# Kernel tuning notes

Measured on AMD Instinct MI355X. Metric: run time of the kernel, lower is better.

## Reference

```python
import jax, jax.numpy as jnp
import numpy as np

DIM = 512
HEADS = 4
MARGIN = 1.0


def _attn_pool(x, Wq, bq, Wk, bk, Wv, bv, Wo, bo):
    # SelfAttention(video_dim, m_dim=DIM, heads=HEADS) followed by mean over time
    B, T, _ = x.shape
    hd = DIM // HEADS
    q = (x @ Wq + bq).reshape(B, T, HEADS, hd)
    k = (x @ Wk + bk).reshape(B, T, HEADS, hd)
    v = (x @ Wv + bv).reshape(B, T, HEADS, hd)
    a = jax.nn.softmax(jnp.einsum('bthd,bshd->bhts', q, k) / jnp.sqrt(jnp.float32(hd)), axis=-1)
    out = jnp.einsum('bhts,bshd->bthd', a, v).reshape(B, T, DIM) @ Wo + bo
    return out.mean(axis=1)  # [B, DIM]


def _ranking(x1, x2, gmask, margin):
    # vectorized form of the per-row torch.roll loop:
    # s[i, b] = <x1[b], x2[(b - i) mod B]>
    B = x1.shape[0]
    idx = (jnp.arange(B)[None, :] - jnp.arange(B)[:, None]) % B  # [B, B]
    s = jnp.einsum('bc,ibc->ib', x1, x2[idx])                    # [B, B]
    mask = gmask[idx] & gmask[None, :]                           # [B, B]
    # max-margin ranking loss with per-column masked mean, then mean over valid cols
    loss = jnp.maximum(0.0, margin + s[1:] - s[0:1])             # [B-1, B]
    m = mask[1:]
    cnt = m.sum(axis=0)
    col_mean = jnp.where(cnt > 0, (loss * m).sum(axis=0) / jnp.maximum(cnt, 1), 0.0)
    valid = cnt > 0
    loss_val = jnp.sum(col_mean * valid) / jnp.maximum(valid.sum(), 1)
    # ranking accuracy: idx==0 iff the true (row 0) score is max among selected
    sel_sum = jnp.sum(jnp.where(mask, s, 0.0), axis=0)
    col_valid = (sel_sum != 0) & mask.any(axis=0)
    s_masked = jnp.where(mask, s, -jnp.inf)
    top_is_first = (s[0] >= s_masked.max(axis=0)).astype(jnp.float32)
    acc = jnp.sum(jnp.where(col_valid, top_is_first, 0.0)) / jnp.maximum(col_valid.sum(), 1)
    return loss_val, jax.lax.stop_gradient(acc)


def setup_inputs() -> dict:
    key = jax.random.key(0)
    ks = iter(jax.random.split(key, 64))

    def nrm(shape, s=0.02):
        return jax.random.normal(next(ks), shape, jnp.float32) * s

    inp = {
        'o': jax.random.normal(next(ks), (128, 1024, DIM), jnp.float32),
        'rgb': jax.random.normal(next(ks), (128, 64, 2048), jnp.float32),
        'audio': jax.random.normal(next(ks), (128, 64, 128), jnp.float32),
        'group_mask': jax.random.randint(next(ks), (128,), 0, 2).astype(bool),
    }
    for name, d in (('rgb', 2048), ('audio', 128)):
        inp[f'{name}_Wq'] = nrm((d, DIM)); inp[f'{name}_bq'] = jnp.zeros((DIM,), jnp.float32)
        inp[f'{name}_Wk'] = nrm((d, DIM)); inp[f'{name}_bk'] = jnp.zeros((DIM,), jnp.float32)
        inp[f'{name}_Wv'] = nrm((d, DIM)); inp[f'{name}_bv'] = jnp.zeros((DIM,), jnp.float32)
        inp[f'{name}_Wo'] = nrm((DIM, DIM)); inp[f'{name}_bo'] = jnp.zeros((DIM,), jnp.float32)
        inp[f'{name}_W2'] = nrm((DIM, DIM)); inp[f'{name}_b2'] = jnp.zeros((DIM,), jnp.float32)
    inp['expand_W'] = nrm((DIM, 2 * DIM))
    inp['expand_b'] = jnp.zeros((2 * DIM,), jnp.float32)
    return inp


def reference(o, rgb, audio, group_mask,
              rgb_Wq, rgb_bq, rgb_Wk, rgb_bk, rgb_Wv, rgb_bv, rgb_Wo, rgb_bo, rgb_W2, rgb_b2,
              audio_Wq, audio_bq, audio_Wk, audio_bk, audio_Wv, audio_bv, audio_Wo, audio_bo,
              audio_W2, audio_b2, expand_W, expand_b):
    # per-modality encoders (CollaborativeGating multiplies are discarded in the
    # original forward, so gating is a no-op on the output -> skipped)
    f_rgb = _attn_pool(rgb, rgb_Wq, rgb_bq, rgb_Wk, rgb_bk, rgb_Wv, rgb_bv, rgb_Wo, rgb_bo) @ rgb_W2 + rgb_b2
    f_aud = _attn_pool(audio, audio_Wq, audio_bq, audio_Wk, audio_bk, audio_Wv, audio_bv, audio_Wo, audio_bo) @ audio_W2 + audio_b2
    feat = jnp.concatenate([f_rgb, f_aud], axis=-1)  # [B, 2*DIM]
    oo = o.mean(axis=-2) @ expand_W + expand_b       # [B, 2*DIM]
    oo = oo / jnp.maximum(jnp.linalg.norm(oo, axis=-1, keepdims=True), 1e-12)
    l1, a1 = _ranking(oo, feat, group_mask, MARGIN)
    l2, a2 = _ranking(feat, oo, group_mask, MARGIN)
    loss = l1 + l2
    acc = (a1 + a2) / 2.0
    return loss, acc
```

## Files before the change

### kernel.cpp

```cpp
#include <hip/hip_runtime.h>
#include <hip/hip_bf16.h>
#include <math.h>


using bf16x8 = __attribute__((ext_vector_type(8))) __bf16;
using f32x4  = __attribute__((ext_vector_type(4))) float;

enum : size_t {
  B_PART = 0,
  B_OM   = B_PART + (size_t)128*32*512*4,
  B_OO   = B_OM   + (size_t)128*512*4,
  B_G    = B_OO   + (size_t)128*1024*4,
  B_PP   = B_G    + (size_t)128*128*4,
  B_PO   = B_PP   + (size_t)2*128*512*4,
  B_FEAT = B_PO   + (size_t)2*128*512*4,
  B_QBF  = B_FEAT + (size_t)2*128*512*4,
  B_KBF  = B_QBF  + (size_t)2*8192*512*2,
  B_VF   = B_KBF  + (size_t)2*8192*512*2,
  B_XBF  = B_VF   + (size_t)2*8192*512*4,
  B_WT   = B_XBF  + (size_t)8192*2048*2,
  B_END  = B_WT   + (size_t)3*512*2048*2
};

__global__ __launch_bounds__(256) void mean_partial_k(const float* __restrict__ o,
                                                      float* __restrict__ part) {
  int c = blockIdx.x, b = blockIdx.y;
  const float* base = o + ((size_t)b * 1024 + (size_t)c * 64) * 512;
  int d4 = (threadIdx.x & 127) << 2;
  int half = threadIdx.x >> 7;
  float4 s = {0.f, 0.f, 0.f, 0.f};
  for (int t = half; t < 64; t += 2) {
    float4 v = *(const float4*)(base + (size_t)t * 512 + d4);
    s.x += v.x; s.y += v.y; s.z += v.z; s.w += v.w;
  }
  *(float4*)(part + (((size_t)b * 16 + c) * 2 + half) * 512 + d4) = s;
}

__global__ __launch_bounds__(512) void finalize_mean_k(const float* __restrict__ part,
                                                       float* __restrict__ om) {
  int b = blockIdx.x, d = threadIdx.x;
  float s = 0.f;
  for (int c = 0; c < 32; ++c) s += part[((size_t)b * 32 + c) * 512 + d];
  om[(size_t)b * 512 + d] = s * (1.f / 1024.f);
}

__global__ __launch_bounds__(256) void gemm_f32_k(
    const float* __restrict__ A, int lda,
    const float* __restrict__ W, int ldw,
    const float* __restrict__ bias,
    float* __restrict__ C, int ldc, int K) {
  __shared__ float As[16][65];
  __shared__ float Ws[16][64];
  int tid = threadIdx.x;
  int tx = tid & 15, ty = tid >> 4;
  int row0 = blockIdx.y * 64, col0 = blockIdx.x * 64;
  float acc[4][4] = {};
  int ar = tid >> 2, ac = (tid & 3) << 2;
  int wr = tid >> 4, wc = (tid & 15) << 2;
  for (int k0 = 0; k0 < K; k0 += 16) {
    float4 av = *(const float4*)(A + (size_t)(row0 + ar) * lda + k0 + ac);
    As[ac + 0][ar] = av.x; As[ac + 1][ar] = av.y;
    As[ac + 2][ar] = av.z; As[ac + 3][ar] = av.w;
    float4 wv = *(const float4*)(W + (size_t)(k0 + wr) * ldw + col0 + wc);
    *(float4*)&Ws[wr][wc] = wv;
    __syncthreads();
#pragma unroll
    for (int k = 0; k < 16; ++k) {
      float a0 = As[k][(ty << 2) + 0], a1 = As[k][(ty << 2) + 1];
      float a2 = As[k][(ty << 2) + 2], a3 = As[k][(ty << 2) + 3];
      float4 w = *(const float4*)&Ws[k][tx << 2];
      acc[0][0] += a0 * w.x; acc[0][1] += a0 * w.y; acc[0][2] += a0 * w.z; acc[0][3] += a0 * w.w;
      acc[1][0] += a1 * w.x; acc[1][1] += a1 * w.y; acc[1][2] += a1 * w.z; acc[1][3] += a1 * w.w;
      acc[2][0] += a2 * w.x; acc[2][1] += a2 * w.y; acc[2][2] += a2 * w.z; acc[2][3] += a2 * w.w;
      acc[3][0] += a3 * w.x; acc[3][1] += a3 * w.y; acc[3][2] += a3 * w.z; acc[3][3] += a3 * w.w;
    }
    __syncthreads();
  }
  float4 bv = *(const float4*)(bias + col0 + (tx << 2));
#pragma unroll
  for (int i = 0; i < 4; ++i) {
    float4 ov;
    ov.x = acc[i][0] + bv.x; ov.y = acc[i][1] + bv.y;
    ov.z = acc[i][2] + bv.z; ov.w = acc[i][3] + bv.w;
    *(float4*)(C + (size_t)(row0 + (ty << 2) + i) * ldc + col0 + (tx << 2)) = ov;
  }
}

__global__ __launch_bounds__(256) void gemm_f32_2w_k(
    const float* __restrict__ A,
    const float* __restrict__ W0, const float* __restrict__ W1,
    const float* __restrict__ b0, const float* __restrict__ b1,
    float* __restrict__ C) {
  const float* W = (blockIdx.y >= 2) ? W1 : W0;
  const float* bias = (blockIdx.y >= 2) ? b1 : b0;
  __shared__ float As[16][65];
  __shared__ float Ws[16][64];
  int tid = threadIdx.x;
  int tx = tid & 15, ty = tid >> 4;
  int row0 = blockIdx.y * 64, col0 = blockIdx.x * 64;
  float acc[4][4] = {};
  int ar = tid >> 2, ac = (tid & 3) << 2;
  int wr = tid >> 4, wc = (tid & 15) << 2;
  for (int k0 = 0; k0 < 512; k0 += 16) {
    float4 av = *(const float4*)(A + (size_t)(row0 + ar) * 512 + k0 + ac);
    As[ac + 0][ar] = av.x; As[ac + 1][ar] = av.y;
    As[ac + 2][ar] = av.z; As[ac + 3][ar] = av.w;
    float4 wv = *(const float4*)(W + (size_t)(k0 + wr) * 512 + col0 + wc);
    *(float4*)&Ws[wr][wc] = wv;
    __syncthreads();
#pragma unroll
    for (int k = 0; k < 16; ++k) {
      float a0 = As[k][(ty << 2) + 0], a1 = As[k][(ty << 2) + 1];
      float a2 = As[k][(ty << 2) + 2], a3 = As[k][(ty << 2) + 3];
      float4 w = *(const float4*)&Ws[k][tx << 2];
      acc[0][0] += a0 * w.x; acc[0][1] += a0 * w.y; acc[0][2] += a0 * w.z; acc[0][3] += a0 * w.w;
      acc[1][0] += a1 * w.x; acc[1][1] += a1 * w.y; acc[1][2] += a1 * w.z; acc[1][3] += a1 * w.w;
      acc[2][0] += a2 * w.x; acc[2][1] += a2 * w.y; acc[2][2] += a2 * w.z; acc[2][3] += a2 * w.w;
      acc[3][0] += a3 * w.x; acc[3][1] += a3 * w.y; acc[3][2] += a3 * w.z; acc[3][3] += a3 * w.w;
    }
    __syncthreads();
  }
  float4 bv = *(const float4*)(bias + col0 + (tx << 2));
#pragma unroll
  for (int i = 0; i < 4; ++i) {
    float4 ov;
    ov.x = acc[i][0] + bv.x; ov.y = acc[i][1] + bv.y;
    ov.z = acc[i][2] + bv.z; ov.w = acc[i][3] + bv.w;
    *(float4*)(C + (size_t)(row0 + (ty << 2) + i) * 512 + col0 + (tx << 2)) = ov;
  }
}

__device__ __forceinline__ unsigned short f2bf(float f) {
  __hip_bfloat16 h = __float2bfloat16(f);
  return __builtin_bit_cast(unsigned short, h);
}

__global__ __launch_bounds__(256) void cast_k(const float* __restrict__ x,
                                              unsigned short* __restrict__ y, int n) {
  int i = (blockIdx.x * 256 + threadIdx.x) * 4;
  int stride = gridDim.x * 1024;
  for (; i < n; i += stride) {
    float4 v = *(const float4*)(x + i);
    ushort4 u;
    u.x = f2bf(v.x); u.y = f2bf(v.y); u.z = f2bf(v.z); u.w = f2bf(v.w);
    *(ushort4*)(y + i) = u;
  }
}

struct W3 { const float* w[3]; unsigned short* wt[3]; };
__global__ void castT3_k(W3 a, int K) {
  const float* W = a.w[blockIdx.z];
  unsigned short* Wt = a.wt[blockIdx.z];
  __shared__ float t[32][33];
  int n0 = blockIdx.x * 32, k0 = blockIdx.y * 32;
  int tx = threadIdx.x, ty = threadIdx.y;
#pragma unroll
  for (int i = 0; i < 4; ++i)
    t[ty + 8 * i][tx] = W[(size_t)(k0 + ty + 8 * i) * 512 + n0 + tx];
  __syncthreads();
#pragma unroll
  for (int i = 0; i < 4; ++i)
    Wt[(size_t)(n0 + ty + 8 * i) * K + k0 + tx] = f2bf(t[tx][ty + 8 * i]);
}

struct QkvArgs {
  const unsigned short* Wt[3];
  const float* bias[3];
  void* out[3];
};

__device__ __forceinline__ void stage16(const void* g, void* l) {
  __builtin_amdgcn_global_load_lds((const __attribute__((address_space(1))) void*)g,
                                   (__attribute__((address_space(3))) void*)l, 16, 0, 0);
}

__global__ __launch_bounds__(256) void gemm_bf16_qkv(
    const unsigned short* __restrict__ A,
    QkvArgs args, int K) {
  __shared__ unsigned short As[128 * 32];
  __shared__ unsigned short Bs[128 * 32];
  int id = blockIdx.x;
  int by = id & 63, bx = (id >> 6) & 3, bz = id >> 8;
  const unsigned short* Bt = args.Wt[bz];
  const float* bias = args.bias[bz];

  int tid = threadIdx.x;
  int l = tid & 63, w = tid >> 6;
  int row0 = by * 128, col0 = bx * 128;
  int wrow = (w & 1) * 64, wcol = (w >> 1) * 64;
  int kg = l >> 4, lr = l & 15;

  f32x4 acc[4][4] = {};

  for (int k0 = 0; k0 < K; k0 += 32) {
#pragma unroll
    for (int i = 0; i < 2; ++i) {
      int c = w * 128 + i * 64 + l;
      int r = c >> 2, s = (c & 3) * 8;
      stage16(A + (size_t)(row0 + r) * K + k0 + s, (char*)As + (size_t)(w * 128 + i * 64) * 16);
      stage16(Bt + (size_t)(col0 + r) * K + k0 + s, (char*)Bs + (size_t)(w * 128 + i * 64) * 16);
    }
    __syncthreads();
    bf16x8 af[4], bfr[4];
#pragma unroll
    for (int m = 0; m < 4; ++m) {
      af[m]  = *(const bf16x8*)(As + (size_t)(wrow + m * 16 + lr) * 32 + kg * 8);
      bfr[m] = *(const bf16x8*)(Bs + (size_t)(wcol + m * 16 + lr) * 32 + kg * 8);
    }
#pragma unroll
    for (int m = 0; m < 4; ++m)
#pragma unroll
      for (int n = 0; n < 4; ++n)
        acc[m][n] = __builtin_amdgcn_mfma_f32_16x16x32_bf16(af[m], bfr[n], acc[m][n], 0, 0, 0);
    __syncthreads();
  }

  int orow = row0 + wrow + kg * 4;
  int ocol = col0 + wcol + lr;
  float bv[4];
#pragma unroll
  for (int n = 0; n < 4; ++n) bv[n] = bias[ocol + n * 16];
  if (bz < 2) {
    unsigned short* C = (unsigned short*)args.out[bz];
#pragma unroll
    for (int m = 0; m < 4; ++m)
#pragma unroll
      for (int n = 0; n < 4; ++n)
#pragma unroll
        for (int j = 0; j < 4; ++j)
          C[(size_t)(orow + m * 16 + j) * 512 + ocol + n * 16] = f2bf(acc[m][n][j] + bv[n]);
  } else {
    float* C = (float*)args.out[2];
#pragma unroll
    for (int m = 0; m < 4; ++m)
#pragma unroll
      for (int n = 0; n < 4; ++n)
#pragma unroll
        for (int j = 0; j < 4; ++j)
          C[(size_t)(orow + m * 16 + j) * 512 + ocol + n * 16] = acc[m][n][j] + bv[n];
  }
}

__global__ __launch_bounds__(256) void attn_pool_mfma_k(
    const unsigned short* __restrict__ qbf,
    const unsigned short* __restrict__ kbf,
    const float* __restrict__ vf,
    float* __restrict__ pooled) {
  __shared__ float wlds[4][64];
  __shared__ float wf[64];
  int h = blockIdx.x, b = blockIdx.y, m = blockIdx.z;
  size_t base = ((size_t)m * 8192 + (size_t)b * 64) * 512 + h * 128;
  int tid = threadIdx.x;
  int w = tid >> 6, l = tid & 63, lr = l & 15, g = l >> 4;

  bf16x8 qf[4];
#pragma unroll
  for (int ks = 0; ks < 4; ++ks)
    qf[ks] = *(const bf16x8*)(qbf + base + (size_t)(16 * w + lr) * 512 + 32 * ks + 8 * g);

  f32x4 accT[4];
#pragma unroll
  for (int tr = 0; tr < 4; ++tr) {
    f32x4 a = {0.f, 0.f, 0.f, 0.f};
#pragma unroll
    for (int ks = 0; ks < 4; ++ks) {
      bf16x8 kfr = *(const bf16x8*)(kbf + base + (size_t)(16 * tr + lr) * 512 + 32 * ks + 8 * g);
      a = __builtin_amdgcn_mfma_f32_16x16x32_bf16(kfr, qf[ks], a, 0, 0, 0);
    }
    accT[tr] = a;
  }

  const float scale = 0.08838834764831845f;
  float p[4][4];
  float lm = -INFINITY;
#pragma unroll
  for (int tr = 0; tr < 4; ++tr)
#pragma unroll
    for (int j = 0; j < 4; ++j) { p[tr][j] = accT[tr][j] * scale; lm = fmaxf(lm, p[tr][j]); }
  lm = fmaxf(lm, __shfl_xor(lm, 16));
  lm = fmaxf(lm, __shfl_xor(lm, 32));
  float ls = 0.f;
#pragma unroll
  for (int tr = 0; tr < 4; ++tr)
#pragma unroll
    for (int j = 0; j < 4; ++j) { p[tr][j] = expf(p[tr][j] - lm); ls += p[tr][j]; }
  ls += __shfl_xor(ls, 16);
  ls += __shfl_xor(ls, 32);
  float inv = 1.f / ls;
#pragma unroll
  for (int tr = 0; tr < 4; ++tr)
#pragma unroll
    for (int j = 0; j < 4; ++j) {
      float c = p[tr][j] * inv;
      c += __shfl_xor(c, 1);
      c += __shfl_xor(c, 2);
      c += __shfl_xor(c, 4);
      c += __shfl_xor(c, 8);
      p[tr][j] = c;
    }
  if (lr == 0) {
#pragma unroll
    for (int tr = 0; tr < 4; ++tr)
#pragma unroll
      for (int j = 0; j < 4; ++j)
        wlds[w][16 * tr + 4 * g + j] = p[tr][j];
  }
  __syncthreads();
  if (tid < 64)
    wf[tid] = (wlds[0][tid] + wlds[1][tid] + wlds[2][tid] + wlds[3][tid]) * (1.f / 64.f);
  __syncthreads();

  int dd = tid & 127, t2 = tid >> 7;
  float ps = 0.f;
  for (int s = t2 * 32; s < t2 * 32 + 32; ++s)
    ps += wf[s] * vf[base + (size_t)s * 512 + dd];
  atomicAdd(&pooled[((size_t)m * 128 + b) * 512 + h * 128 + dd], ps);
}

__global__ __launch_bounds__(256) void l2norm_k(float* __restrict__ x, int C) {
  int b = blockIdx.x;
  float* row = x + (size_t)b * C;
  int tid = threadIdx.x;
  float ss = 0.f;
  for (int c = tid; c < C; c += 256) { float v = row[c]; ss += v * v; }
#pragma unroll
  for (int off = 32; off >= 1; off >>= 1) ss += __shfl_down(ss, off);
  __shared__ float wsum[4];
  if ((tid & 63) == 0) wsum[tid >> 6] = ss;
  __syncthreads();
  float total = wsum[0] + wsum[1] + wsum[2] + wsum[3];
  float inv = 1.f / fmaxf(sqrtf(total), 1e-12f);
  for (int c = tid; c < C; c += 256) row[c] *= inv;
}

__global__ __launch_bounds__(256) void gemm_nt_k(const float* __restrict__ A,
                                                 const float* __restrict__ Bsplit,
                                                 float* __restrict__ G) {
  __shared__ float As[16][68];
  __shared__ float Bs[16][68];
  int tid = threadIdx.x, tx = tid & 15, ty = tid >> 4;
  int row0 = blockIdx.y * 64, col0 = blockIdx.x * 64;
  float acc[4][4] = {};
  int ar = tid >> 2, ac = (tid & 3) << 2;
  for (int k0 = 0; k0 < 1024; k0 += 16) {
    float4 av = *(const float4*)(A + (size_t)(row0 + ar) * 1024 + k0 + ac);
    As[ac + 0][ar] = av.x; As[ac + 1][ar] = av.y;
    As[ac + 2][ar] = av.z; As[ac + 3][ar] = av.w;
    float4 bv = *(const float4*)(Bsplit + (size_t)((k0 >> 9) * 128 + col0 + ar) * 512 + (k0 & 511) + ac);
    Bs[ac + 0][ar] = bv.x; Bs[ac + 1][ar] = bv.y;
    Bs[ac + 2][ar] = bv.z; Bs[ac + 3][ar] = bv.w;
    __syncthreads();
#pragma unroll
    for (int k = 0; k < 16; ++k) {
      float4 a4 = *(const float4*)&As[k][ty << 2];
      float4 b4 = *(const float4*)&Bs[k][tx << 2];
      acc[0][0] += a4.x * b4.x; acc[0][1] += a4.x * b4.y; acc[0][2] += a4.x * b4.z; acc[0][3] += a4.x * b4.w;
      acc[1][0] += a4.y * b4.x; acc[1][1] += a4.y * b4.y; acc[1][2] += a4.y * b4.z; acc[1][3] += a4.y * b4.w;
      acc[2][0] += a4.z * b4.x; acc[2][1] += a4.z * b4.y; acc[2][2] += a4.z * b4.z; acc[2][3] += a4.z * b4.w;
      acc[3][0] += a4.w * b4.x; acc[3][1] += a4.w * b4.y; acc[3][2] += a4.w * b4.z; acc[3][3] += a4.w * b4.w;
    }
    __syncthreads();
  }
#pragma unroll
  for (int i = 0; i < 4; ++i)
    *(float4*)(G + (size_t)(row0 + (ty << 2) + i) * 128 + col0 + (tx << 2)) = *(float4*)acc[i];
}

__global__ __launch_bounds__(128) void final_k(const float* __restrict__ G,
                                               const int* __restrict__ gmask,
                                               float* __restrict__ out) {
  __shared__ float cm[2][128], vd[2][128], tp[2][128], cv[2][128];
  __shared__ int gm[128];
  int b = threadIdx.x;
  gm[b] = gmask[b];
  __syncthreads();
  for (int r = 0; r < 2; ++r) {
    bool gb = gm[b] != 0;
    float s0 = G[b * 128 + b];
    int cnt = 0;
    float lsum = 0.f, selsum = 0.f, smax = -INFINITY;
    bool anym = false;
    for (int i = 0; i < 128; ++i) {
      int j = (b - i + 128) & 127;
      bool mk = gb && (gm[j] != 0);
      float sv = (r == 0) ? G[b * 128 + j] : G[j * 128 + b];
      if (mk) {
        selsum += sv; anym = true;
        smax = fmaxf(smax, sv);
        if (i >= 1) { cnt++; lsum += fmaxf(0.f, 1.f + sv - s0); }
      }
    }
    cm[r][b] = (cnt > 0) ? (lsum / (float)cnt) : 0.f;
    vd[r][b] = (cnt > 0) ? 1.f : 0.f;
    bool colvalid = (selsum != 0.f) && anym;
    tp[r][b] = (colvalid && (s0 >= smax)) ? 1.f : 0.f;
    cv[r][b] = colvalid ? 1.f : 0.f;
  }
  __syncthreads();
  if (b == 0) {
    float loss = 0.f, acc = 0.f;
    for (int r = 0; r < 2; ++r) {
      float scm = 0, svd = 0, stp = 0, scv = 0;
      for (int i = 0; i < 128; ++i) { scm += cm[r][i]; svd += vd[r][i]; stp += tp[r][i]; scv += cv[r][i]; }
      loss += scm / fmaxf(svd, 1.f);
      acc += stp / fmaxf(scv, 1.f);
    }
    out[0] = loss;
    out[1] = acc * 0.5f;
  }
}

extern "C" void kernel_launch(void* const* d_in, const int* in_sizes, int n_in,
                              void* d_out, int out_size, void* d_ws, size_t ws_size,
                              hipStream_t stream) {
  const float* o     = (const float*)d_in[0];
  const float* rgb   = (const float*)d_in[1];
  const float* audio = (const float*)d_in[2];
  const int* gmask   = (const int*)d_in[3];
  const float* W[2][10];
  for (int m = 0; m < 2; ++m)
    for (int w = 0; w < 10; ++w) W[m][w] = (const float*)d_in[4 + m * 10 + w];
  const float* expand_W = (const float*)d_in[24];
  const float* expand_b = (const float*)d_in[25];

  char* ws = (char*)d_ws;
  float* part = (float*)(ws + B_PART);
  float* om   = (float*)(ws + B_OM);
  float* oo   = (float*)(ws + B_OO);
  float* G    = (float*)(ws + B_G);
  float* pp2  = (float*)(ws + B_PP);
  float* po2  = (float*)(ws + B_PO);
  float* feat2= (float*)(ws + B_FEAT);
  unsigned short* qbf = (unsigned short*)(ws + B_QBF);
  unsigned short* kbf = (unsigned short*)(ws + B_KBF);
  float* vf   = (float*)(ws + B_VF);
  unsigned short* xbf = (unsigned short*)(ws + B_XBF);
  unsigned short* wt0 = (unsigned short*)(ws + B_WT);
  unsigned short* wt1 = wt0 + (size_t)512 * 2048;
  unsigned short* wt2 = wt1 + (size_t)512 * 2048;

  mean_partial_k<<<dim3(16, 128), 256, 0, stream>>>(o, part);
  finalize_mean_k<<<128, 512, 0, stream>>>(part, om);
  gemm_f32_k<<<dim3(16, 2), 256, 0, stream>>>(om, 512, expand_W, 1024, expand_b, oo, 1024, 512);
  l2norm_k<<<128, 256, 0, stream>>>(oo, 1024);

  const float* Xs[2] = {rgb, audio};
  const int Ks[2] = {2048, 128};
  for (int m = 0; m < 2; ++m) {
    int K = Ks[m];
    cast_k<<<dim3(m == 0 ? 2048 : 512), 256, 0, stream>>>(Xs[m], xbf, 8192 * K);
    W3 w3;
    w3.w[0] = W[m][0]; w3.w[1] = W[m][2]; w3.w[2] = W[m][4];
    w3.wt[0] = wt0; w3.wt[1] = wt1; w3.wt[2] = wt2;
    castT3_k<<<dim3(16, K / 32, 3), dim3(32, 8), 0, stream>>>(w3, K);
    QkvArgs args;
    args.Wt[0] = wt0; args.Wt[1] = wt1; args.Wt[2] = wt2;
    args.bias[0] = W[m][1]; args.bias[1] = W[m][3]; args.bias[2] = W[m][5];
    args.out[0] = qbf + (size_t)m * 8192 * 512;
    args.out[1] = kbf + (size_t)m * 8192 * 512;
    args.out[2] = vf + (size_t)m * 8192 * 512;
    gemm_bf16_qkv<<<768, 256, 0, stream>>>(xbf, args, K);
  }

  hipMemsetAsync(pp2, 0, 2 * 128 * 512 * sizeof(float), stream);
  attn_pool_mfma_k<<<dim3(4, 128, 2), 256, 0, stream>>>(qbf, kbf, vf, pp2);

  gemm_f32_2w_k<<<dim3(8, 4), 256, 0, stream>>>(pp2, W[0][6], W[1][6], W[0][7], W[1][7], po2);
  gemm_f32_2w_k<<<dim3(8, 4), 256, 0, stream>>>(po2, W[0][8], W[1][8], W[0][9], W[1][9], feat2);

  gemm_nt_k<<<dim3(2, 2), 256, 0, stream>>>(oo, feat2, G);
  final_k<<<1, 128, 0, stream>>>(G, gmask, (float*)d_out);
}
```

Baseline: 411.5 us.

## Fuse launches across pipeline: single prep, merged QKV, fused attention-pool and projections

Cuts the number of kernel launches throughout the pipeline. The mean reduction becomes a single kernel. The casts and weight transposes for both modalities run in one prep kernel, and both QKV GEMMs run in one launch. Attention pooling handles all heads per block, so the atomics and the memset go away. The two projection GEMMs are fused with a bf16 intermediate, and the l2norm is folded into the Gram GEMM. The main cost targeted is launch overhead and serialisation; the trade-offs are less rounding fidelity in the projection and some grids with low parallelism (32 blocks in pofeat).

```diff
diff --git a/kernel.cpp b/kernel.cpp
--- a/kernel.cpp
+++ b/kernel.cpp
@@ -7,41 +7,43 @@
 using f32x4  = __attribute__((ext_vector_type(4))) float;
 
 enum : size_t {
-  B_PART = 0,
-  B_OM   = B_PART + (size_t)128*32*512*4,
+  B_OM   = 0,
   B_OO   = B_OM   + (size_t)128*512*4,
   B_G    = B_OO   + (size_t)128*1024*4,
   B_PP   = B_G    + (size_t)128*128*4,
-  B_PO   = B_PP   + (size_t)2*128*512*4,
-  B_FEAT = B_PO   + (size_t)2*128*512*4,
+  B_FEAT = B_PP   + (size_t)2*128*512*4,
   B_QBF  = B_FEAT + (size_t)2*128*512*4,
   B_KBF  = B_QBF  + (size_t)2*8192*512*2,
   B_VF   = B_KBF  + (size_t)2*8192*512*2,
-  B_XBF  = B_VF   + (size_t)2*8192*512*4,
-  B_WT   = B_XBF  + (size_t)8192*2048*2,
-  B_END  = B_WT   + (size_t)3*512*2048*2
+  B_XR   = B_VF   + (size_t)2*8192*512*4,
+  B_XA   = B_XR   + (size_t)8192*2048*2,
+  B_WT   = B_XA   + (size_t)8192*128*2,
+  B_END  = B_WT   + (size_t)3*512*2048*2 + (size_t)3*512*128*2
 };
 
-__global__ __launch_bounds__(256) void mean_partial_k(const float* __restrict__ o,
-                                                      float* __restrict__ part) {
-  int c = blockIdx.x, b = blockIdx.y;
-  const float* base = o + ((size_t)b * 1024 + (size_t)c * 64) * 512;
-  int d4 = (threadIdx.x & 127) << 2;
-  int half = threadIdx.x >> 7;
+__device__ __forceinline__ unsigned short f2bf(float f) {
+  __hip_bfloat16 h = __float2bfloat16(f);
+  return __builtin_bit_cast(unsigned short, h);
+}
+__device__ __forceinline__ float bf2f(unsigned short u) {
+  return __builtin_bit_cast(float, (unsigned)u << 16);
+}
+
+__global__ __launch_bounds__(512) void mean_k(const float* __restrict__ o,
+                                              float* __restrict__ om) {
+  __shared__ float part[4][512];
+  int b = blockIdx.x, tid = threadIdx.x;
+  int d4 = (tid & 127) << 2, tg = tid >> 7;
+  const float* base = o + (size_t)b * 1024 * 512;
   float4 s = {0.f, 0.f, 0.f, 0.f};
-  for (int t = half; t < 64; t += 2) {
+  for (int t = tg; t < 1024; t += 4) {
     float4 v = *(const float4*)(base + (size_t)t * 512 + d4);
     s.x += v.x; s.y += v.y; s.z += v.z; s.w += v.w;
   }
-  *(float4*)(part + (((size_t)b * 16 + c) * 2 + half) * 512 + d4) = s;
-}
-
-__global__ __launch_bounds__(512) void finalize_mean_k(const float* __restrict__ part,
-                                                       float* __restrict__ om) {
-  int b = blockIdx.x, d = threadIdx.x;
-  float s = 0.f;
-  for (int c = 0; c < 32; ++c) s += part[((size_t)b * 32 + c) * 512 + d];
-  om[(size_t)b * 512 + d] = s * (1.f / 1024.f);
+  *(float4*)&part[tg][d4] = s;
+  __syncthreads();
+  float r = part[0][tid] + part[1][tid] + part[2][tid] + part[3][tid];
+  om[(size_t)b * 512 + tid] = r * (1.f / 1024.f);
 }
 
 __global__ __launch_bounds__(256) void gemm_f32_k(
@@ -86,74 +88,18 @@
   }
 }
 
-__global__ __launch_bounds__(256) void gemm_f32_2w_k(
-    const float* __restrict__ A,
-    const float* __restrict__ W0, const float* __restrict__ W1,
-    const float* __restrict__ b0, const float* __restrict__ b1,
-    float* __restrict__ C) {
-  const float* W = (blockIdx.y >= 2) ? W1 : W0;
-  const float* bias = (blockIdx.y >= 2) ? b1 : b0;
-  __shared__ float As[16][65];
-  __shared__ float Ws[16][64];
-  int tid = threadIdx.x;
-  int tx = tid & 15, ty = tid >> 4;
-  int row0 = blockIdx.y * 64, col0 = blockIdx.x * 64;
-  float acc[4][4] = {};
-  int ar = tid >> 2, ac = (tid & 3) << 2;
-  int wr = tid >> 4, wc = (tid & 15) << 2;
-  for (int k0 = 0; k0 < 512; k0 += 16) {
-    float4 av = *(const float4*)(A + (size_t)(row0 + ar) * 512 + k0 + ac);
-    As[ac + 0][ar] = av.x; As[ac + 1][ar] = av.y;
-    As[ac + 2][ar] = av.z; As[ac + 3][ar] = av.w;
-    float4 wv = *(const float4*)(W + (size_t)(k0 + wr) * 512 + col0 + wc);
-    *(float4*)&Ws[wr][wc] = wv;
-    __syncthreads();
-#pragma unroll
-    for (int k = 0; k < 16; ++k) {
-      float a0 = As[k][(ty << 2) + 0], a1 = As[k][(ty << 2) + 1];
-      float a2 = As[k][(ty << 2) + 2], a3 = As[k][(ty << 2) + 3];
-      float4 w = *(const float4*)&Ws[k][tx << 2];
-      acc[0][0] += a0 * w.x; acc[0][1] += a0 * w.y; acc[0][2] += a0 * w.z; acc[0][3] += a0 * w.w;
-      acc[1][0] += a1 * w.x; acc[1][1] += a1 * w.y; acc[1][2] += a1 * w.z; acc[1][3] += a1 * w.w;
-      acc[2][0] += a2 * w.x; acc[2][1] += a2 * w.y; acc[2][2] += a2 * w.z; acc[2][3] += a2 * w.w;
-      acc[3][0] += a3 * w.x; acc[3][1] += a3 * w.y; acc[3][2] += a3 * w.z; acc[3][3] += a3 * w.w;
-    }
-    __syncthreads();
-  }
-  float4 bv = *(const float4*)(bias + col0 + (tx << 2));
-#pragma unroll
-  for (int i = 0; i < 4; ++i) {
-    float4 ov;
-    ov.x = acc[i][0] + bv.x; ov.y = acc[i][1] + bv.y;
-    ov.z = acc[i][2] + bv.z; ov.w = acc[i][3] + bv.w;
-    *(float4*)(C + (size_t)(row0 + (ty << 2) + i) * 512 + col0 + (tx << 2)) = ov;
-  }
-}
-
-__device__ __forceinline__ unsigned short f2bf(float f) {
-  __hip_bfloat16 h = __float2bfloat16(f);
-  return __builtin_bit_cast(unsigned short, h);
-}
-
-__global__ __launch_bounds__(256) void cast_k(const float* __restrict__ x,
-                                              unsigned short* __restrict__ y, int n) {
-  int i = (blockIdx.x * 256 + threadIdx.x) * 4;
-  int stride = gridDim.x * 1024;
-  for (; i < n; i += stride) {
-    float4 v = *(const float4*)(x + i);
-    ushort4 u;
-    u.x = f2bf(v.x); u.y = f2bf(v.y); u.z = f2bf(v.z); u.w = f2bf(v.w);
-    *(ushort4*)(y + i) = u;
-  }
-}
-
-struct W3 { const float* w[3]; unsigned short* wt[3]; };
-__global__ void castT3_k(W3 a, int K) {
-  const float* W = a.w[blockIdx.z];
-  unsigned short* Wt = a.wt[blockIdx.z];
+struct PrepArgs {
+  const float* xr; unsigned short* xrb;
+  const float* xa; unsigned short* xab;
+  const float* w[6];
+  unsigned short* wt[6];
+};
+
+__device__ __forceinline__ void transpose_cast_tile(
+    const float* __restrict__ W, unsigned short* __restrict__ Wt,
+    int K, int n0, int k0, int tid) {
   __shared__ float t[32][33];
-  int n0 = blockIdx.x * 32, k0 = blockIdx.y * 32;
-  int tx = threadIdx.x, ty = threadIdx.y;
+  int tx = tid & 31, ty = tid >> 5;
 #pragma unroll
   for (int i = 0; i < 4; ++i)
     t[ty + 8 * i][tx] = W[(size_t)(k0 + ty + 8 * i) * 512 + n0 + tx];
@@ -163,10 +109,37 @@
     Wt[(size_t)(n0 + ty + 8 * i) * K + k0 + tx] = f2bf(t[tx][ty + 8 * i]);
 }
 
-struct QkvArgs {
-  const unsigned short* Wt[3];
-  const float* bias[3];
-  void* out[3];
+__device__ __forceinline__ void cast_range(const float* __restrict__ x,
+                                           unsigned short* __restrict__ y,
+                                           int i, int stride, int total) {
+  for (; i < total; i += stride) {
+    float4 v = *(const float4*)(x + (size_t)i * 4);
+    ushort4 u;
+    u.x = f2bf(v.x); u.y = f2bf(v.y); u.z = f2bf(v.z); u.w = f2bf(v.w);
+    *(ushort4*)(y + (size_t)i * 4) = u;
+  }
+}
+
+__global__ __launch_bounds__(256) void prep_k(PrepArgs a) {
+  int bid = blockIdx.x, tid = threadIdx.x;
+  if (bid < 3072) {
+    int w = bid >> 10, t = bid & 1023;
+    transpose_cast_tile(a.w[w], a.wt[w], 2048, (t & 15) * 32, (t >> 4) * 32, tid);
+  } else if (bid < 3264) {
+    int t = bid - 3072; int w = t >> 6; t &= 63;
+    transpose_cast_tile(a.w[3 + w], a.wt[3 + w], 128, (t & 15) * 32, (t >> 4) * 32, tid);
+  } else if (bid < 5312) {
+    cast_range(a.xr, a.xrb, (bid - 3264) * 256 + tid, 524288, 4194304);
+  } else {
+    cast_range(a.xa, a.xab, (bid - 5312) * 256 + tid, 32768, 262144);
+  }
+}
+
+struct QkvAll {
+  const unsigned short* A[2];
+  const unsigned short* Wt[6];
+  const float* bias[6];
+  void* out[6];
 };
 
 __device__ __forceinline__ void stage16(const void* g, void* l) {
@@ -174,15 +147,17 @@
                                    (__attribute__((address_space(3))) void*)l, 16, 0, 0);
 }
 
-__global__ __launch_bounds__(256) void gemm_bf16_qkv(
-    const unsigned short* __restrict__ A,
-    QkvArgs args, int K) {
-  __shared__ unsigned short As[128 * 32];
-  __shared__ unsigned short Bs[128 * 32];
+__global__ __launch_bounds__(256) void qkv_k(QkvAll args) {
+  __shared__ __align__(16) unsigned short As[128 * 32];
+  __shared__ __align__(16) unsigned short Bs[128 * 32];
   int id = blockIdx.x;
+  int mi = id >= 768 ? 1 : 0; id -= mi * 768;
   int by = id & 63, bx = (id >> 6) & 3, bz = id >> 8;
-  const unsigned short* Bt = args.Wt[bz];
-  const float* bias = args.bias[bz];
+  int K = mi ? 128 : 2048;
+  const unsigned short* A = args.A[mi];
+  int wi = mi * 3 + bz;
+  const unsigned short* Bt = args.Wt[wi];
+  const float* bias = args.bias[wi];
 
   int tid = threadIdx.x;
   int l = tid & 63, w = tid >> 6;
@@ -221,7 +196,7 @@
 #pragma unroll
   for (int n = 0; n < 4; ++n) bv[n] = bias[ocol + n * 16];
   if (bz < 2) {
-    unsigned short* C = (unsigned short*)args.out[bz];
+    unsigned short* C = (unsigned short*)args.out[wi];
 #pragma unroll
     for (int m = 0; m < 4; ++m)
 #pragma unroll
@@ -230,7 +205,7 @@
         for (int j = 0; j < 4; ++j)
           C[(size_t)(orow + m * 16 + j) * 512 + ocol + n * 16] = f2bf(acc[m][n][j] + bv[n]);
   } else {
-    float* C = (float*)args.out[2];
+    float* C = (float*)args.out[wi];
 #pragma unroll
     for (int m = 0; m < 4; ++m)
 #pragma unroll
@@ -241,129 +216,204 @@
   }
 }
 
-__global__ __launch_bounds__(256) void attn_pool_mfma_k(
+__global__ __launch_bounds__(256) void attn_pool_k(
     const unsigned short* __restrict__ qbf,
     const unsigned short* __restrict__ kbf,
     const float* __restrict__ vf,
     float* __restrict__ pooled) {
   __shared__ float wlds[4][64];
-  __shared__ float wf[64];
-  int h = blockIdx.x, b = blockIdx.y, m = blockIdx.z;
-  size_t base = ((size_t)m * 8192 + (size_t)b * 64) * 512 + h * 128;
+  int b = blockIdx.x, m = blockIdx.y;
   int tid = threadIdx.x;
   int w = tid >> 6, l = tid & 63, lr = l & 15, g = l >> 4;
-
-  bf16x8 qf[4];
-#pragma unroll
-  for (int ks = 0; ks < 4; ++ks)
-    qf[ks] = *(const bf16x8*)(qbf + base + (size_t)(16 * w + lr) * 512 + 32 * ks + 8 * g);
-
-  f32x4 accT[4];
-#pragma unroll
-  for (int tr = 0; tr < 4; ++tr) {
-    f32x4 a = {0.f, 0.f, 0.f, 0.f};
-#pragma unroll
-    for (int ks = 0; ks < 4; ++ks) {
-      bf16x8 kfr = *(const bf16x8*)(kbf + base + (size_t)(16 * tr + lr) * 512 + 32 * ks + 8 * g);
-      a = __builtin_amdgcn_mfma_f32_16x16x32_bf16(kfr, qf[ks], a, 0, 0, 0);
-    }
-    accT[tr] = a;
+  size_t base = ((size_t)m * 8192 + (size_t)b * 64) * 512 + w * 128;
+
+  bf16x8 qf[4][4];
+#pragma unroll
+  for (int tb = 0; tb < 4; ++tb)
+#pragma unroll
+    for (int ks = 0; ks < 4; ++ks)
+      qf[tb][ks] = *(const bf16x8*)(qbf + base + (size_t)(tb * 16 + lr) * 512 + ks * 32 + g * 8);
+
+  f32x4 acc[4][4] = {};
+#pragma unroll
+  for (int sb = 0; sb < 4; ++sb) {
+    bf16x8 kf[4];
+#pragma unroll
+    for (int ks = 0; ks < 4; ++ks)
+      kf[ks] = *(const bf16x8*)(kbf + base + (size_t)(sb * 16 + lr) * 512 + ks * 32 + g * 8);
+#pragma unroll
+    for (int tb = 0; tb < 4; ++tb)
+#pragma unroll
+      for (int ks = 0; ks < 4; ++ks)
+        acc[sb][tb] = __builtin_amdgcn_mfma_f32_16x16x32_bf16(kf[ks], qf[tb][ks], acc[sb][tb], 0, 0, 0);
   }
 
   const float scale = 0.08838834764831845f;
-  float p[4][4];
-  float lm = -INFINITY;
-#pragma unroll
-  for (int tr = 0; tr < 4; ++tr)
-#pragma unroll
-    for (int j = 0; j < 4; ++j) { p[tr][j] = accT[tr][j] * scale; lm = fmaxf(lm, p[tr][j]); }
-  lm = fmaxf(lm, __shfl_xor(lm, 16));
-  lm = fmaxf(lm, __shfl_xor(lm, 32));
-  float ls = 0.f;
-#pragma unroll
-  for (int tr = 0; tr < 4; ++tr)
-#pragma unroll
-    for (int j = 0; j < 4; ++j) { p[tr][j] = expf(p[tr][j] - lm); ls += p[tr][j]; }
-  ls += __shfl_xor(ls, 16);
-  ls += __shfl_xor(ls, 32);
-  float inv = 1.f / ls;
-#pragma unroll
-  for (int tr = 0; tr < 4; ++tr)
+  float mx[4] = {-INFINITY, -INFINITY, -INFINITY, -INFINITY};
+#pragma unroll
+  for (int sb = 0; sb < 4; ++sb)
+#pragma unroll
+    for (int tb = 0; tb < 4; ++tb)
+#pragma unroll
+      for (int j = 0; j < 4; ++j) {
+        acc[sb][tb][j] *= scale;
+        mx[tb] = fmaxf(mx[tb], acc[sb][tb][j]);
+      }
+#pragma unroll
+  for (int tb = 0; tb < 4; ++tb) {
+    mx[tb] = fmaxf(mx[tb], __shfl_xor(mx[tb], 16));
+    mx[tb] = fmaxf(mx[tb], __shfl_xor(mx[tb], 32));
+  }
+  float sm[4] = {0.f, 0.f, 0.f, 0.f};
+#pragma unroll
+  for (int sb = 0; sb < 4; ++sb)
+#pragma unroll
+    for (int tb = 0; tb < 4; ++tb)
+#pragma unroll
+      for (int j = 0; j < 4; ++j) {
+        float e = expf(acc[sb][tb][j] - mx[tb]);
+        acc[sb][tb][j] = e;
+        sm[tb] += e;
+      }
+  float inv[4];
+#pragma unroll
+  for (int tb = 0; tb < 4; ++tb) {
+    sm[tb] += __shfl_xor(sm[tb], 16);
+    sm[tb] += __shfl_xor(sm[tb], 32);
+    inv[tb] = 1.f / sm[tb];
+  }
+#pragma unroll
+  for (int sb = 0; sb < 4; ++sb)
 #pragma unroll
     for (int j = 0; j < 4; ++j) {
-      float c = p[tr][j] * inv;
-      c += __shfl_xor(c, 1);
-      c += __shfl_xor(c, 2);
-      c += __shfl_xor(c, 4);
-      c += __shfl_xor(c, 8);
-      p[tr][j] = c;
-    }
-  if (lr == 0) {
-#pragma unroll
-    for (int tr = 0; tr < 4; ++tr)
-#pragma unroll
-      for (int j = 0; j < 4; ++j)
-        wlds[w][16 * tr + 4 * g + j] = p[tr][j];
-  }
+      float cs = acc[sb][0][j] * inv[0] + acc[sb][1][j] * inv[1]
+               + acc[sb][2][j] * inv[2] + acc[sb][3][j] * inv[3];
+      cs += __shfl_xor(cs, 1);
+      cs += __shfl_xor(cs, 2);
+      cs += __shfl_xor(cs, 4);
+      cs += __shfl_xor(cs, 8);
+      if (lr == 0) wlds[w][sb * 16 + g * 4 + j] = cs * (1.f / 64.f);
+    }
   __syncthreads();
-  if (tid < 64)
-    wf[tid] = (wlds[0][tid] + wlds[1][tid] + wlds[2][tid] + wlds[3][tid]) * (1.f / 64.f);
+
+  int h = tid >> 6, c2 = (tid & 63) << 1;
+  size_t vbase = ((size_t)m * 8192 + (size_t)b * 64) * 512 + h * 128 + c2;
+  float s0 = 0.f, s1 = 0.f;
+#pragma unroll 8
+  for (int s = 0; s < 64; ++s) {
+    float2 v = *(const float2*)(vf + vbase + (size_t)s * 512);
+    float wv = wlds[h][s];
+    s0 += wv * v.x; s1 += wv * v.y;
+  }
+  float2 o2 = {s0, s1};
+  *(float2*)(pooled + ((size_t)m * 128 + b) * 512 + h * 128 + c2) = o2;
+}
+
+__global__ __launch_bounds__(256) void pofeat_k(
+    const float* __restrict__ pp,
+    const float* __restrict__ Wo0, const float* __restrict__ bo0,
+    const float* __restrict__ W20, const float* __restrict__ b20,
+    const float* __restrict__ Wo1, const float* __restrict__ bo1,
+    const float* __restrict__ W21, const float* __restrict__ b21,
+    float* __restrict__ feat) {
+  __shared__ __align__(16) float Ws[16][512];
+  __shared__ unsigned short po[8][512];
+  __shared__ float As[8][16];
+  int m = blockIdx.y, rb = blockIdx.x;
+  const float* Wo = m ? Wo1 : Wo0;
+  const float* bo = m ? bo1 : bo0;
+  const float* W2 = m ? W21 : W20;
+  const float* b2 = m ? b21 : b20;
+  int row0 = m * 128 + rb * 8;
+  int tid = threadIdx.x;
+  int r = tid >> 5, tx = tid & 31;
+
+  float acc[16];
+#pragma unroll
+  for (int j = 0; j < 16; ++j) acc[j] = 0.f;
+  for (int k0 = 0; k0 < 512; k0 += 16) {
+    __syncthreads();
+#pragma unroll
+    for (int i = 0; i < 8; ++i) {
+      int idx = (i * 256 + tid) * 4;
+      *(float4*)&Ws[idx >> 9][idx & 511] =
+          *(const float4*)(Wo + (size_t)(k0 + (idx >> 9)) * 512 + (idx & 511));
+    }
+    if (tid < 128) As[tid >> 4][tid & 15] = pp[(size_t)(row0 + (tid >> 4)) * 512 + k0 + (tid & 15)];
+    __syncthreads();
+#pragma unroll
+    for (int k = 0; k < 16; ++k) {
+      float a = As[r][k];
+#pragma unroll
+      for (int j = 0; j < 16; ++j) acc[j] += a * Ws[k][tx + 32 * j];
+    }
+  }
+#pragma unroll
+  for (int j = 0; j < 16; ++j) po[r][tx + 32 * j] = f2bf(acc[j] + bo[tx + 32 * j]);
+
+#pragma unroll
+  for (int j = 0; j < 16; ++j) acc[j] = 0.f;
+  for (int k0 = 0; k0 < 512; k0 += 16) {
+    __syncthreads();
+#pragma unroll
+    for (int i = 0; i < 8; ++i) {
+      int idx = (i * 256 + tid) * 4;
+      *(float4*)&Ws[idx >> 9][idx & 511] =
+          *(const float4*)(W2 + (size_t)(k0 + (idx >> 9)) * 512 + (idx & 511));
+    }
+    __syncthreads();
+#pragma unroll
+    for (int k = 0; k < 16; ++k) {
+      float a = bf2f(po[r][k0 + k]);
+#pragma unroll
+      for (int j = 0; j < 16; ++j) acc[j] += a * Ws[k][tx + 32 * j];
+    }
+  }
+#pragma unroll
+  for (int j = 0; j < 16; ++j)
+    feat[(size_t)(row0 + r) * 512 + tx + 32 * j] = acc[j] + b2[tx + 32 * j];
+}
+
+__global__ __launch_bounds__(256) void ntg_k(const float* __restrict__ oo,
+                                             const float* __restrict__ feat,
+                                             float* __restrict__ G) {
+  __shared__ float As[16][33], Bs[16][33];
+  __shared__ float inv32[32];
+  int tid = threadIdx.x;
+  int row0 = blockIdx.y * 32, col0 = blockIdx.x * 32;
+  int ar = tid >> 3, aq = tid & 7;
+  int ty = tid >> 4, tx = tid & 15;
+  float acc[2][2] = {};
+  float ssq = 0.f;
+  for (int k0 = 0; k0 < 1024; k0 += 16) {
+    float2 av = *(const float2*)(oo + (size_t)(row0 + ar) * 1024 + k0 + aq * 2);
+    As[aq * 2 + 0][ar] = av.x;
+    As[aq * 2 + 1][ar] = av.y;
+    ssq += av.x * av.x + av.y * av.y;
+    int kk = k0 + aq * 2;
+    float2 bv = *(const float2*)(feat + (size_t)((kk >> 9) * 128 + col0 + ar) * 512 + (kk & 511));
+    Bs[aq * 2 + 0][ar] = bv.x;
+    Bs[aq * 2 + 1][ar] = bv.y;
+    __syncthreads();
+#pragma unroll
+    for (int k = 0; k < 16; ++k) {
+      float a0 = As[k][ty * 2], a1 = As[k][ty * 2 + 1];
+      float b0 = Bs[k][tx * 2], b1 = Bs[k][tx * 2 + 1];
+      acc[0][0] += a0 * b0; acc[0][1] += a0 * b1;
+      acc[1][0] += a1 * b0; acc[1][1] += a1 * b1;
+    }
+    __syncthreads();
+  }
+  ssq += __shfl_xor(ssq, 1);
+  ssq += __shfl_xor(ssq, 2);
+  ssq += __shfl_xor(ssq, 4);
+  if (aq == 0) inv32[ar] = 1.f / fmaxf(sqrtf(ssq), 1e-12f);
   __syncthreads();
-
-  int dd = tid & 127, t2 = tid >> 7;
-  float ps = 0.f;
-  for (int s = t2 * 32; s < t2 * 32 + 32; ++s)
-    ps += wf[s] * vf[base + (size_t)s * 512 + dd];
-  atomicAdd(&pooled[((size_t)m * 128 + b) * 512 + h * 128 + dd], ps);
-}
-
-__global__ __launch_bounds__(256) void l2norm_k(float* __restrict__ x, int C) {
-  int b = blockIdx.x;
-  float* row = x + (size_t)b * C;
-  int tid = threadIdx.x;
-  float ss = 0.f;
-  for (int c = tid; c < C; c += 256) { float v = row[c]; ss += v * v; }
-#pragma unroll
-  for (int off = 32; off >= 1; off >>= 1) ss += __shfl_down(ss, off);
-  __shared__ float wsum[4];
-  if ((tid & 63) == 0) wsum[tid >> 6] = ss;
-  __syncthreads();
-  float total = wsum[0] + wsum[1] + wsum[2] + wsum[3];
-  float inv = 1.f / fmaxf(sqrtf(total), 1e-12f);
-  for (int c = tid; c < C; c += 256) row[c] *= inv;
-}
-
-__global__ __launch_bounds__(256) void gemm_nt_k(const float* __restrict__ A,
-                                                 const float* __restrict__ Bsplit,
-                                                 float* __restrict__ G) {
-  __shared__ float As[16][68];
-  __shared__ float Bs[16][68];
-  int tid = threadIdx.x, tx = tid & 15, ty = tid >> 4;
-  int row0 = blockIdx.y * 64, col0 = blockIdx.x * 64;
-  float acc[4][4] = {};
-  int ar = tid >> 2, ac = (tid & 3) << 2;
-  for (int k0 = 0; k0 < 1024; k0 += 16) {
-    float4 av = *(const float4*)(A + (size_t)(row0 + ar) * 1024 + k0 + ac);
-    As[ac + 0][ar] = av.x; As[ac + 1][ar] = av.y;
-    As[ac + 2][ar] = av.z; As[ac + 3][ar] = av.w;
-    float4 bv = *(const float4*)(Bsplit + (size_t)((k0 >> 9) * 128 + col0 + ar) * 512 + (k0 & 511) + ac);
-    Bs[ac + 0][ar] = bv.x; Bs[ac + 1][ar] = bv.y;
-    Bs[ac + 2][ar] = bv.z; Bs[ac + 3][ar] = bv.w;
-    __syncthreads();
-#pragma unroll
-    for (int k = 0; k < 16; ++k) {
-      float4 a4 = *(const float4*)&As[k][ty << 2];
-      float4 b4 = *(const float4*)&Bs[k][tx << 2];
-      acc[0][0] += a4.x * b4.x; acc[0][1] += a4.x * b4.y; acc[0][2] += a4.x * b4.z; acc[0][3] += a4.x * b4.w;
-      acc[1][0] += a4.y * b4.x; acc[1][1] += a4.y * b4.y; acc[1][2] += a4.y * b4.z; acc[1][3] += a4.y * b4.w;
-      acc[2][0] += a4.z * b4.x; acc[2][1] += a4.z * b4.y; acc[2][2] += a4.z * b4.z; acc[2][3] += a4.z * b4.w;
-      acc[3][0] += a4.w * b4.x; acc[3][1] += a4.w * b4.y; acc[3][2] += a4.w * b4.z; acc[3][3] += a4.w * b4.w;
-    }
-    __syncthreads();
-  }
-#pragma unroll
-  for (int i = 0; i < 4; ++i)
-    *(float4*)(G + (size_t)(row0 + (ty << 2) + i) * 128 + col0 + (tx << 2)) = *(float4*)acc[i];
+#pragma unroll
+  for (int i = 0; i < 2; ++i)
+#pragma unroll
+    for (int j = 0; j < 2; ++j)
+      G[(size_t)(row0 + ty * 2 + i) * 128 + col0 + tx * 2 + j] = acc[i][j] * inv32[ty * 2 + i];
 }
 
 __global__ __launch_bounds__(128) void final_k(const float* __restrict__ G,
@@ -424,50 +474,51 @@
   const float* expand_b = (const float*)d_in[25];
 
   char* ws = (char*)d_ws;
-  float* part = (float*)(ws + B_PART);
   float* om   = (float*)(ws + B_OM);
   float* oo   = (float*)(ws + B_OO);
   float* G    = (float*)(ws + B_G);
   float* pp2  = (float*)(ws + B_PP);
-  float* po2  = (float*)(ws + B_PO);
   float* feat2= (float*)(ws + B_FEAT);
   unsigned short* qbf = (unsigned short*)(ws + B_QBF);
   unsigned short* kbf = (unsigned short*)(ws + B_KBF);
   float* vf   = (float*)(ws + B_VF);
-  unsigned short* xbf = (unsigned short*)(ws + B_XBF);
-  unsigned short* wt0 = (unsigned short*)(ws + B_WT);
-  unsigned short* wt1 = wt0 + (size_t)512 * 2048;
-  unsigned short* wt2 = wt1 + (size_t)512 * 2048;
-
-  mean_partial_k<<<dim3(16, 128), 256, 0, stream>>>(o, part);
-  finalize_mean_k<<<128, 512, 0, stream>>>(part, om);
+  unsigned short* xrb = (unsigned short*)(ws + B_XR);
+  unsigned short* xab = (unsigned short*)(ws + B_XA);
+  unsigned short* wt  = (unsigned short*)(ws + B_WT);
+  unsigned short* wtp[6];
+  wtp[0] = wt;
+  wtp[1] = wtp[0] + (size_t)512 * 2048;
+  wtp[2] = wtp[1] + (size_t)512 * 2048;
+  wtp[3] = wtp[2] + (size_t)512 * 2048;
+  wtp[4] = wtp[3] + (size_t)512 * 128;
+  wtp[5] = wtp[4] + (size_t)512 * 128;
+
+  mean_k<<<128, 512, 0, stream>>>(o, om);
   gemm_f32_k<<<dim3(16, 2), 256, 0, stream>>>(om, 512, expand_W, 1024, expand_b, oo, 1024, 512);
-  l2norm_k<<<128, 256, 0, stream>>>(oo, 1024);
-
-  const float* Xs[2] = {rgb, audio};
-  const int Ks[2] = {2048, 128};
-  for (int m = 0; m < 2; ++m) {
-    int K = Ks[m];
-    cast_k<<<dim3(m == 0 ? 2048 : 512), 256, 0, stream>>>(Xs[m], xbf, 8192 * K);
-    W3 w3;
-    w3.w[0] = W[m][0]; w3.w[1] = W[m][2]; w3.w[2] = W[m][4];
-    w3.wt[0] = wt0; w3.wt[1] = wt1; w3.wt[2] = wt2;
-    castT3_k<<<dim3(16, K / 32, 3), dim3(32, 8), 0, stream>>>(w3, K);
-    QkvArgs args;
-    args.Wt[0] = wt0; args.Wt[1] = wt1; args.Wt[2] = wt2;
-    args.bias[0] = W[m][1]; args.bias[1] = W[m][3]; args.bias[2] = W[m][5];
-    args.out[0] = qbf + (size_t)m * 8192 * 512;
-    args.out[1] = kbf + (size_t)m * 8192 * 512;
-    args.out[2] = vf + (size_t)m * 8192 * 512;
-    gemm_bf16_qkv<<<768, 256, 0, stream>>>(xbf, args, K);
-  }
-
-  hipMemsetAsync(pp2, 0, 2 * 128 * 512 * sizeof(float), stream);
-  attn_pool_mfma_k<<<dim3(4, 128, 2), 256, 0, stream>>>(qbf, kbf, vf, pp2);
-
-  gemm_f32_2w_k<<<dim3(8, 4), 256, 0, stream>>>(pp2, W[0][6], W[1][6], W[0][7], W[1][7], po2);
-  gemm_f32_2w_k<<<dim3(8, 4), 256, 0, stream>>>(po2, W[0][8], W[1][8], W[0][9], W[1][9], feat2);
-
-  gemm_nt_k<<<dim3(2, 2), 256, 0, stream>>>(oo, feat2, G);
+
+  PrepArgs pa;
+  pa.xr = rgb;   pa.xrb = xrb;
+  pa.xa = audio; pa.xab = xab;
+  pa.w[0] = W[0][0]; pa.w[1] = W[0][2]; pa.w[2] = W[0][4];
+  pa.w[3] = W[1][0]; pa.w[4] = W[1][2]; pa.w[5] = W[1][4];
+  for (int i = 0; i < 6; ++i) pa.wt[i] = wtp[i];
+  prep_k<<<5440, 256, 0, stream>>>(pa);
+
+  QkvAll qa;
+  qa.A[0] = xrb; qa.A[1] = xab;
+  for (int i = 0; i < 6; ++i) qa.Wt[i] = wtp[i];
+  qa.bias[0] = W[0][1]; qa.bias[1] = W[0][3]; qa.bias[2] = W[0][5];
+  qa.bias[3] = W[1][1]; qa.bias[4] = W[1][3]; qa.bias[5] = W[1][5];
+  qa.out[0] = qbf;                       qa.out[1] = kbf;                       qa.out[2] = vf;
+  qa.out[3] = qbf + (size_t)8192 * 512;  qa.out[4] = kbf + (size_t)8192 * 512;  qa.out[5] = vf + (size_t)8192 * 512;
+  qkv_k<<<1536, 256, 0, stream>>>(qa);
+
+  attn_pool_k<<<dim3(128, 2), 256, 0, stream>>>(qbf, kbf, vf, pp2);
+
+  pofeat_k<<<dim3(16, 2), 256, 0, stream>>>(pp2,
+      W[0][6], W[0][7], W[0][8], W[0][9],
+      W[1][6], W[1][7], W[1][8], W[1][9], feat2);
+
+  ntg_k<<<dim3(4, 4), 256, 0, stream>>>(oo, feat2, G);
   final_k<<<1, 128, 0, stream>>>(G, gmask, (float*)d_out);
 }
```

Result: slower. 522.0 us (+26.9%).
